# Performance work log

Hardware: AMD Instinct MI355X
Metric: run time of the kernel (lower is better)

Reference implementation:

```python
import jax, jax.numpy as jnp
import numpy as np

B, L, Hp, N, E, Z, GC = 32, 512, 192, 512, 128, 64, 3
TEMP, ALPHA, EPS = 0.5, 0.5, 1e-10


def _reparam(k, mu, var):
    return mu + jax.random.normal(k, mu.shape, mu.dtype) * jnp.exp(0.5 * var)


def setup_inputs() -> dict:
    key = jax.random.key(0)
    ks = jax.random.split(key, 42)
    def W(i, shape):
        return jax.random.normal(ks[i], shape, jnp.float32) * 0.02
    return {
        "batch_x": jax.random.normal(ks[0], (B, L, N), jnp.float32),
        "time_x": jax.random.normal(ks[1], (B, L, 7), jnp.float32),
        "time_W": W(2, (7, E)), "time_b": W(3, (E,)),
        "gate_W": W(4, (L, N)), "gate_b": W(5, (N,)),
        "mu_t_W": W(6, (E, Z)), "mu_t_b": W(7, (Z,)),
        "var_t_W": W(8, (E, Z)), "var_t_b": W(9, (Z,)),
        "ser_W": W(10, (L, E)), "ser_b": W(11, (E,)),
        "mu_h_W": W(12, (E, Z)), "mu_h_b": W(13, (Z,)),
        "var_h_W": W(14, (E, Z)), "var_h_b": W(15, (Z,)),
        "wkey": W(16, (Z, 1)), "wquery": W(17, (Z, 1)),
        "mlp_W": W(18, (GC + 1, 1)), "mlp_b": W(19, (1,)),
        "mu_ht_W": W(20, (E, Z)), "mu_ht_b": W(21, (Z,)),
        "var_ht_W": W(22, (E, Z)), "var_ht_b": W(23, (Z,)),
        "inf_W": W(24, (Z, Z)), "inf_b": W(25, (Z,)),
        "mu_zt_W": W(26, (Z, Z)), "mu_zt_b": W(27, (Z,)),
        "var_zt_W": W(28, (Z, Z)), "var_zt_b": W(29, (Z,)),
        "fW1": W(30, (Z, E)), "fb1": W(31, (E,)),
        "fW2": W(32, (E, Hp)), "fb2": W(33, (Hp,)),
        "rW1": W(34, (Z, E)), "rb1": W(35, (E,)),
        "rW2": W(36, (E, L)), "rb2": W(37, (L,)),
        "is_eval": 1,
    }


def _forward(batch_x, time_x, time_W, time_b, gate_W, gate_b, mu_t_W, mu_t_b,
             var_t_W, var_t_b, ser_W, ser_b, mu_h_W, mu_h_b, var_h_W, var_h_b,
             wkey, wquery, mlp_W, mlp_b, mu_ht_W, mu_ht_b, var_ht_W, var_ht_b,
             inf_W, inf_b, mu_zt_W, mu_zt_b, var_zt_W, var_zt_b,
             fW1, fb1, fW2, fb2, rW1, rb1, rW2, rb2):
    kz1, kz2, kg = jax.random.split(jax.random.key(42), 3)
    # TimeFeatureEmbedding + gate_layer_0 (Linear over the L axis)
    t = time_x @ time_W + time_b                                   # [B,L,E]
    t = jnp.einsum('ble,ln->bne', t, gate_W) + gate_b[None, :, None]  # [B,N,E]
    mu_t = t @ mu_t_W + mu_t_b
    var_t = t @ var_t_W + var_t_b
    # SeriesEmbedding: per-series Linear L->E, fused with time embedding
    h = jnp.einsum('bln,le->bne', batch_x, ser_W) + ser_b          # [B,N,E]
    h_hat = h + t
    mu_h_hat = h_hat @ mu_h_W + mu_h_b
    var_h_hat = h_hat @ var_h_W + var_h_b
    z_hat = _reparam(kz1, mu_h_hat, var_h_hat)                     # [B,N,Z]
    # self_graph_attention: key/query outer-sum -> leakyrelu -> softmax
    ksc = (z_hat @ wkey)[..., 0]                                   # [B,N]
    qsc = (z_hat @ wquery)[..., 0]
    att = jax.nn.softmax(jax.nn.leaky_relu(ksc[:, :, None] + qsc[:, None, :], 0.2), axis=-1)
    # (dropout identity in eval mode)
    lg = (att + 1.0) / 2.0                                         # [B,N,N]
    lg2 = jnp.stack([lg, 1.0 - lg], axis=-1).reshape(N * N, -1)    # [N*N, 2B] (faithful torch reshape)
    g = -jnp.log(-jnp.log(jax.random.uniform(kg, lg2.shape, lg2.dtype) + EPS) + EPS)
    soft = jax.nn.softmax((lg2 + g) / TEMP, axis=-1)
    hard = jax.nn.one_hot(jnp.argmax(soft, axis=-1), soft.shape[-1], dtype=soft.dtype)
    adj = (jax.lax.stop_gradient(hard - soft) + soft)[:, 0].reshape(N, N)
    adj = adj * (1.0 - jnp.eye(N, dtype=adj.dtype))                # masked_fill diagonal
    # graph_convolution: einsum('bnd,nn->bnd') takes the DIAGONAL of adj (faithful)
    diag = jnp.diagonal(adj)
    Hc, outs = h_hat, [h_hat]
    for _ in range(GC):
        Hc = Hc * diag[None, :, None]
        outs.append(Hc)
    h_tilde = (jnp.stack(outs, axis=-1) @ mlp_W + mlp_b)[..., 0]   # [B,N,E]
    mu_ht = h_tilde @ mu_ht_W + mu_ht_b
    var_ht = h_tilde @ var_ht_W + var_ht_b
    z_tilde = _reparam(kz2, mu_ht, var_ht)
    z = ALPHA * z_hat + (1.0 - ALPHA) * z_tilde
    mu_z = ALPHA * mu_h_hat + (1.0 - ALPHA) * mu_ht
    var_z = ALPHA * var_h_hat + (1.0 - ALPHA) * var_ht
    zt = z @ inf_W + inf_b
    mu_zt = zt @ mu_zt_W + mu_zt_b
    var_zt = zt @ var_zt_W + var_zt_b
    y = jnp.transpose((jax.nn.leaky_relu(z @ fW1 + fb1, 0.01) + h) @ fW2 + fb2, (0, 2, 1))  # [B,H,N]
    x = jnp.transpose((jax.nn.leaky_relu(z @ rW1 + rb1, 0.01) + h) @ rW2 + rb2, (0, 2, 1))  # [B,L,N]
    return (x, y, mu_t, var_t, mu_zt, var_zt, mu_z, var_z)


def reference(batch_x, time_x, time_W, time_b, gate_W, gate_b, mu_t_W, mu_t_b,
              var_t_W, var_t_b, ser_W, ser_b, mu_h_W, mu_h_b, var_h_W, var_h_b,
              wkey, wquery, mlp_W, mlp_b, mu_ht_W, mu_ht_b, var_ht_W, var_ht_b,
              inf_W, inf_b, mu_zt_W, mu_zt_b, var_zt_W, var_zt_b,
              fW1, fb1, fW2, fb2, rW1, rb1, rW2, rb2, is_eval):
    # is_eval: both branches of discrete_graph call gumbel_softmax(hard=True)
    return _forward(batch_x, time_x, time_W, time_b, gate_W, gate_b, mu_t_W, mu_t_b,
                    var_t_W, var_t_b, ser_W, ser_b, mu_h_W, mu_h_b, var_h_W, var_h_b,
                    wkey, wquery, mlp_W, mlp_b, mu_ht_W, mu_ht_b, var_ht_W, var_ht_b,
                    inf_W, inf_b, mu_zt_W, mu_zt_b, var_zt_W, var_zt_b,
                    fW1, fb1, fW2, fb2, rW1, rb1, rW2, rb2)
```

## Files before the change

### kernel.cpp

```cpp
#include <hip/hip_runtime.h>
#include <cstdint>
#include <cstddef>

#define B_ 32
#define L_ 512
#define HP_ 192
#define N_ 512
#define E_ 128
#define Z_ 64

typedef short bf16x8 __attribute__((ext_vector_type(8)));
typedef float f32x4 __attribute__((ext_vector_type(4)));

__host__ __device__ __forceinline__ uint32_t rotl32(uint32_t v, int r) {
    return (v << r) | (v >> (32 - r));
}

__host__ __device__ __forceinline__ void tf2x32(uint32_t k0, uint32_t k1,
                                                uint32_t c0, uint32_t c1,
                                                uint32_t& o0, uint32_t& o1) {
    uint32_t ks2 = k0 ^ k1 ^ 0x1BD11BDAu;
    uint32_t x0 = c0 + k0, x1 = c1 + k1;
    x0 += x1; x1 = rotl32(x1, 13); x1 ^= x0;
    x0 += x1; x1 = rotl32(x1, 15); x1 ^= x0;
    x0 += x1; x1 = rotl32(x1, 26); x1 ^= x0;
    x0 += x1; x1 = rotl32(x1, 6);  x1 ^= x0;
    x0 += k1; x1 += ks2 + 1u;
    x0 += x1; x1 = rotl32(x1, 17); x1 ^= x0;
    x0 += x1; x1 = rotl32(x1, 29); x1 ^= x0;
    x0 += x1; x1 = rotl32(x1, 16); x1 ^= x0;
    x0 += x1; x1 = rotl32(x1, 24); x1 ^= x0;
    x0 += ks2; x1 += k0 + 2u;
    x0 += x1; x1 = rotl32(x1, 13); x1 ^= x0;
    x0 += x1; x1 = rotl32(x1, 15); x1 ^= x0;
    x0 += x1; x1 = rotl32(x1, 26); x1 ^= x0;
    x0 += x1; x1 = rotl32(x1, 6);  x1 ^= x0;
    x0 += k0; x1 += k1 + 3u;
    x0 += x1; x1 = rotl32(x1, 17); x1 ^= x0;
    x0 += x1; x1 = rotl32(x1, 29); x1 ^= x0;
    x0 += x1; x1 = rotl32(x1, 16); x1 ^= x0;
    x0 += x1; x1 = rotl32(x1, 24); x1 ^= x0;
    x0 += k1; x1 += ks2 + 4u;
    x0 += x1; x1 = rotl32(x1, 13); x1 ^= x0;
    x0 += x1; x1 = rotl32(x1, 15); x1 ^= x0;
    x0 += x1; x1 = rotl32(x1, 26); x1 ^= x0;
    x0 += x1; x1 = rotl32(x1, 6);  x1 ^= x0;
    x0 += ks2; x1 += k0 + 5u;
    o0 = x0; o1 = x1;
}

__device__ __forceinline__ float erfinv_f(float x) {
    float w = -log1pf(-x * x);
    float p;
    if (w < 5.0f) {
        w = w - 2.5f;
        p = 2.81022636e-08f;
        p = fmaf(p, w, 3.43273939e-07f);
        p = fmaf(p, w, -3.5233877e-06f);
        p = fmaf(p, w, -4.39150654e-06f);
        p = fmaf(p, w, 0.00021858087f);
        p = fmaf(p, w, -0.00125372503f);
        p = fmaf(p, w, -0.00417768164f);
        p = fmaf(p, w, 0.246640727f);
        p = fmaf(p, w, 1.50140941f);
    } else {
        w = sqrtf(w) - 3.0f;
        p = -0.000200214257f;
        p = fmaf(p, w, 0.000100950558f);
        p = fmaf(p, w, 0.00134934322f);
        p = fmaf(p, w, -0.00367342844f);
        p = fmaf(p, w, 0.00573950773f);
        p = fmaf(p, w, -0.0076224613f);
        p = fmaf(p, w, 0.00943887047f);
        p = fmaf(p, w, 1.00167406f);
        p = fmaf(p, w, 2.83297682f);
    }
    return p * x;
}

__device__ __forceinline__ float bits_to_normal(uint32_t bits) {
    float f = __uint_as_float((bits >> 9) | 0x3f800000u) - 1.0f;
    const float lo = -0.99999994f;
    float u = fmaxf(lo, f * 2.0f + lo);
    return 1.41421354f * erfinv_f(u);
}

__device__ __forceinline__ uint32_t f2bf1(float x) {
    uint32_t u = __float_as_uint(x);
    return (u + 0x7fffu + ((u >> 16) & 1u)) >> 16;
}
__device__ __forceinline__ uint32_t f2bf2(float lo, float hi) {
    return f2bf1(lo) | (f2bf1(hi) << 16);
}

union U4BF8 { uint4 u; bf16x8 v; };

#define PO_WT   0
#define PO_WH   16384
#define PO_WI   49152
#define PO_WZZ  53248
#define PO_W1F  61440
#define PO_W1R  69632
#define PO_W2F  77824
#define PO_W2R  102400

struct PrepSrcs { const float* p[13]; };

__global__ void k_prep(PrepSrcs S, short* pool) {
    static const int Kt[13]  = {128,128,128,128,128,128,64,64,64,64,64,128,128};
    static const int Nst[13] = {64,64,64,64,64,64,64,64,64,128,128,192,512};
    static const int Ndt[13] = {128,128,256,256,256,256,64,128,128,128,128,192,512};
    static const int c0t[13] = {0,64,0,64,128,192,0,0,64,0,0,0,0};
    static const int offt[13]= {PO_WT,PO_WT,PO_WH,PO_WH,PO_WH,PO_WH,PO_WI,
                                PO_WZZ,PO_WZZ,PO_W1F,PO_W1R,PO_W2F,PO_W2R};
    int j = blockIdx.y;
    int Ns = Nst[j];
    int total = Kt[j] * Ns;
    int idx = blockIdx.x * 256 + threadIdx.x;
    if (idx >= total) return;
    int k = idx / Ns, nc = idx - k * Ns;
    float v = S.p[j][idx];
    int kc = k >> 5, k32 = k & 31;
    int fg = (k32 >> 2) & 3, e = (k32 & 3) + ((k32 >> 4) << 2);
    pool[offt[j] + (size_t)((kc * 4 + fg) * Ndt[j] + c0t[j] + nc) * 8 + e] = (short)f2bf1(v);
}

__global__ void k_pack(const float* __restrict__ gW, const float* __restrict__ sW,
                       const float* __restrict__ tx, const float* __restrict__ tW,
                       const float* __restrict__ tb,
                       const float* __restrict__ mW, const float* __restrict__ vW,
                       short* __restrict__ gfp, short* __restrict__ swp,
                       short* __restrict__ t0p, float* __restrict__ csum) {
    int mode = blockIdx.y;
    int idx = blockIdx.x * 256 + threadIdx.x;
    if (mode == 0) {
        if (idx >= 32768) return;
        int n = idx & 511, r = idx >> 9;
        int kc = r >> 2, fg = r & 3;
        int lb = kc * 32 + fg * 4;
        float v[8];
#pragma unroll
        for (int j = 0; j < 8; ++j)
            v[j] = gW[(size_t)(lb + (j & 3) + ((j >> 2) << 4)) * N_ + n];
        U4BF8 u;
        u.u.x = f2bf2(v[0], v[1]); u.u.y = f2bf2(v[2], v[3]);
        u.u.z = f2bf2(v[4], v[5]); u.u.w = f2bf2(v[6], v[7]);
        *(uint4*)&gfp[(size_t)((((n >> 5) * 16 + kc) * 4 + fg) * 32 + (n & 31)) * 8] = u.u;
    } else if (mode == 1) {
        if (idx >= 8192) return;
        int e = idx & 127, r = idx >> 7;
        int kc = r >> 2, fg = r & 3;
        int lb = kc * 32 + fg * 4;
        float v[8];
#pragma unroll
        for (int j = 0; j < 8; ++j)
            v[j] = sW[(size_t)(lb + (j & 3) + ((j >> 2) << 4)) * E_ + e];
        U4BF8 u;
        u.u.x = f2bf2(v[0], v[1]); u.u.y = f2bf2(v[2], v[3]);
        u.u.z = f2bf2(v[4], v[5]); u.u.w = f2bf2(v[6], v[7]);
        *(uint4*)&swp[(size_t)(r * 128 + e) * 8] = u.u;
    } else if (mode == 2) {
        if (idx >= 262144) return;
        int e = idx & 127, r2 = idx >> 7;
        int b = r2 >> 6, kf = r2 & 63;
        int kc = kf >> 2, fg = kf & 3;
        int lb = kc * 32 + fg * 4;
        float tbe = tb[e];
        float twc[7];
#pragma unroll
        for (int k = 0; k < 7; ++k) twc[k] = tW[k * E_ + e];
        float v[8];
#pragma unroll
        for (int j = 0; j < 8; ++j) {
            int l = lb + (j & 3) + ((j >> 2) << 4);
            const float* txr = &tx[((size_t)b * L_ + l) * 7];
            float a = tbe;
#pragma unroll
            for (int k = 0; k < 7; ++k) a = fmaf(txr[k], twc[k], a);
            v[j] = a;
        }
        U4BF8 u;
        u.u.x = f2bf2(v[0], v[1]); u.u.y = f2bf2(v[2], v[3]);
        u.u.z = f2bf2(v[4], v[5]); u.u.w = f2bf2(v[6], v[7]);
        *(uint4*)&t0p[(size_t)(r2 * 128 + e) * 8] = u.u;
    } else {
        if (idx >= 128) return;
        const float* W = (idx < 64) ? mW : vW;
        int zc = idx & 63;
        float s = 0.0f;
        for (int e = 0; e < E_; ++e) s += W[e * Z_ + zc];
        csum[idx] = s;
    }
}

__global__ __launch_bounds__(256) void k_gate4(
    const float* __restrict__ bx,
    const short* __restrict__ gfp, const short* __restrict__ swp,
    const short* __restrict__ t0p,
    const float* __restrict__ gb, const float* __restrict__ sb,
    float* __restrict__ t, float* __restrict__ h, float* __restrict__ hh) {
    const int ntile = blockIdx.x, eh = blockIdx.y, b = blockIdx.z;
    const int tid = threadIdx.x, lane = tid & 63, wv = tid >> 6;
    const int mw = wv & 1, ew = wv >> 1;
    const int fm = lane & 15, fl = lane >> 4;
    const int n0 = ntile * 32;
    const int e0 = eh * 64 + ew * 32;
    const int n = n0 + mw * 16 + fm;
    const float* bxp = &bx[(size_t)b * L_ * N_ + n];

    const f32x4 z4 = {0.f, 0.f, 0.f, 0.f};
    f32x4 accT[2] = {z4, z4}, accH[2] = {z4, z4};

    for (int kc = 0; kc < 16; ++kc) {
        int lb = kc * 32 + fl * 4;
        float xv[8];
#pragma unroll
        for (int j = 0; j < 8; ++j)
            xv[j] = bxp[(size_t)(lb + (j & 3) + ((j >> 2) << 4)) * N_];
        U4BF8 ux;
        ux.u.x = f2bf2(xv[0], xv[1]); ux.u.y = f2bf2(xv[2], xv[3]);
        ux.u.z = f2bf2(xv[4], xv[5]); ux.u.w = f2bf2(xv[6], xv[7]);
        bf16x8 fbx = ux.v;
        bf16x8 fgw = *(const bf16x8*)&gfp[(size_t)(((ntile * 16 + kc) * 4 + fl) * 32 + mw * 16 + fm) * 8];
#pragma unroll
        for (int nt = 0; nt < 2; ++nt) {
            int ec = e0 + nt * 16 + fm;
            bf16x8 ft = *(const bf16x8*)&t0p[(size_t)(((b * 16 + kc) * 4 + fl) * 128 + ec) * 8];
            bf16x8 fs = *(const bf16x8*)&swp[(size_t)((kc * 4 + fl) * 128 + ec) * 8];
            accT[nt] = __builtin_amdgcn_mfma_f32_16x16x32_bf16(fgw, ft, accT[nt], 0, 0, 0);
            accH[nt] = __builtin_amdgcn_mfma_f32_16x16x32_bf16(fbx, fs, accH[nt], 0, 0, 0);
        }
    }
    float gbn[4];
#pragma unroll
    for (int r = 0; r < 4; ++r) gbn[r] = gb[n0 + mw * 16 + fl * 4 + r];
#pragma unroll
    for (int nt = 0; nt < 2; ++nt) {
        int e = e0 + nt * 16 + fm;
        float sbe = sb[e];
#pragma unroll
        for (int r = 0; r < 4; ++r) {
            int nr = n0 + mw * 16 + fl * 4 + r;
            size_t base = ((size_t)b * N_ + nr) * E_ + e;
            float tv = accT[nt][r] + gbn[r];
            float hv = accH[nt][r] + sbe;
            t[base] = tv; h[base] = hv; hh[base] = tv + hv;
        }
    }
}

__global__ __launch_bounds__(256) void k_mega2(
    const float* __restrict__ T, const float* __restrict__ HH,
    const float* __restrict__ h,
    const short* __restrict__ pool,
    const float* __restrict__ bmt_, const float* __restrict__ bvt_,
    const float* __restrict__ bmh, const float* __restrict__ bvh,
    const float* __restrict__ bmht, const float* __restrict__ bvht,
    const float* __restrict__ mlpW, const float* __restrict__ mlpb,
    const float* __restrict__ csum,
    const float* __restrict__ ib,
    const float* __restrict__ mzb, const float* __restrict__ vzb,
    const float* __restrict__ fb1, const float* __restrict__ rb1,
    float* __restrict__ Omt, float* __restrict__ Ovt,
    float* __restrict__ Omz, float* __restrict__ Ovz,
    float* __restrict__ Omzt, float* __restrict__ Ovzt,
    float* __restrict__ tmpF, float* __restrict__ tmpR,
    uint32_t k1a, uint32_t k1b, uint32_t k2a, uint32_t k2b) {
    __shared__ __align__(16) short sAT[4 * 4 * 32 * 8];
    __shared__ __align__(16) short sAH[4 * 4 * 32 * 8];
    __shared__ __align__(16) short sZf[2 * 4 * 32 * 8];
    __shared__ __align__(16) short sZTf[2 * 4 * 32 * 8];
    __shared__ float sOut[32][260];

    const short* Wt  = pool + PO_WT;
    const short* Wh  = pool + PO_WH;
    const short* Wi  = pool + PO_WI;
    const short* Wzz = pool + PO_WZZ;
    const short* W1f = pool + PO_W1F;
    const short* W1r = pool + PO_W1R;

    const int r0 = blockIdx.x * 32;
    const int tid = threadIdx.x;
    const int lane = tid & 63, wv = tid >> 6;
    const int fm = lane & 15, flane = lane >> 4;
    const int m = wv & 1, nb = wv >> 1;
    const f32x4 z4 = {0.f, 0.f, 0.f, 0.f};

#pragma unroll
    for (int it = 0; it < 4; ++it) {
        int idx = tid + it * 256;
        int row = idx >> 5, c4 = idx & 31;
        int k0 = c4 * 4;
        int kc = k0 >> 5, k32 = k0 & 31;
        int fg = (k32 >> 2) & 3, e0 = (k32 >= 16) ? 4 : 0;
        int base = ((kc * 4 + fg) * 32 + row) * 8 + e0;
        float4 v = *(const float4*)&T[(size_t)(r0 + row) * E_ + k0];
        uint2 u; u.x = f2bf2(v.x, v.y); u.y = f2bf2(v.z, v.w);
        *(uint2*)&sAT[base] = u;
        float4 w = *(const float4*)&HH[(size_t)(r0 + row) * E_ + k0];
        uint2 p; p.x = f2bf2(w.x, w.y); p.y = f2bf2(w.z, w.w);
        *(uint2*)&sAH[base] = p;
    }
    __syncthreads();

    {
        bf16x8 fa[4];
#pragma unroll
        for (int kc = 0; kc < 4; ++kc)
            fa[kc] = *(const bf16x8*)&sAT[((kc * 4 + flane) * 32 + m * 16 + fm) * 8];
        f32x4 acc[4] = {z4, z4, z4, z4};
#pragma unroll
        for (int j = 0; j < 4; ++j) {
            int nt = nb + 2 * j;
#pragma unroll
            for (int kc = 0; kc < 4; ++kc) {
                bf16x8 fb = *(const bf16x8*)&Wt[(size_t)((kc * 4 + flane) * 128 + nt * 16 + fm) * 8];
                acc[j] = __builtin_amdgcn_mfma_f32_16x16x32_bf16(fa[kc], fb, acc[j], 0, 0, 0);
            }
        }
#pragma unroll
        for (int j = 0; j < 4; ++j) {
            int ncol = (nb + 2 * j) * 16 + fm;
            float* dst = (ncol < 64) ? Omt : Ovt;
            int zc = ncol & 63;
            float bias = (ncol < 64) ? bmt_[zc] : bvt_[zc];
#pragma unroll
            for (int r = 0; r < 4; ++r) {
                int row = m * 16 + flane * 4 + r;
                dst[(size_t)(r0 + row) * Z_ + zc] = acc[j][r] + bias;
            }
        }
    }

    {
        bf16x8 fa[4];
#pragma unroll
        for (int kc = 0; kc < 4; ++kc)
            fa[kc] = *(const bf16x8*)&sAH[((kc * 4 + flane) * 32 + m * 16 + fm) * 8];
        f32x4 acc[8] = {z4, z4, z4, z4, z4, z4, z4, z4};
#pragma unroll
        for (int j = 0; j < 8; ++j) {
            int nt = nb + 2 * j;
#pragma unroll
            for (int kc = 0; kc < 4; ++kc) {
                bf16x8 fb = *(const bf16x8*)&Wh[(size_t)((kc * 4 + flane) * 256 + nt * 16 + fm) * 8];
                acc[j] = __builtin_amdgcn_mfma_f32_16x16x32_bf16(fa[kc], fb, acc[j], 0, 0, 0);
            }
        }
#pragma unroll
        for (int j = 0; j < 8; ++j) {
            int ncol = (nb + 2 * j) * 16 + fm;
#pragma unroll
            for (int r = 0; r < 4; ++r)
                sOut[m * 16 + flane * 4 + r][ncol] = acc[j][r];
        }
    }
    __syncthreads();

    {
        float w0 = mlpW[0], b0 = mlpb[0];
        int row = tid >> 3;
        int zc0 = (tid & 7) * 8;
        int r = r0 + row;
        float zm[8], zvv[8];
        uint32_t zb[8];
#pragma unroll
        for (int j = 0; j < 8; ++j) {
            int zc = zc0 + j;
            float m1 = sOut[row][zc] + bmh[zc];
            float v1 = sOut[row][64 + zc] + bvh[zc];
            float m2 = fmaf(w0, sOut[row][128 + zc], fmaf(b0, csum[zc], bmht[zc]));
            float v2 = fmaf(w0, sOut[row][192 + zc], fmaf(b0, csum[64 + zc], bvht[zc]));
            uint32_t flat = (uint32_t)r * 64u + (uint32_t)zc;
            uint32_t o0, o1;
            tf2x32(k1a, k1b, 0u, flat, o0, o1);
            float e1 = bits_to_normal(o0 ^ o1);
            tf2x32(k2a, k2b, 0u, flat, o0, o1);
            float e2 = bits_to_normal(o0 ^ o1);
            float zh = m1 + e1 * expf(0.5f * v1);
            float zt = m2 + e2 * expf(0.5f * v2);
            float zval = 0.5f * (zh + zt);
            zb[j] = f2bf1(zval);
            zm[j] = 0.5f * (m1 + m2);
            zvv[j] = 0.5f * (v1 + v2);
        }
        size_t base = (size_t)r * Z_ + zc0;
        *(float4*)&Omz[base]     = make_float4(zm[0], zm[1], zm[2], zm[3]);
        *(float4*)&Omz[base + 4] = make_float4(zm[4], zm[5], zm[6], zm[7]);
        *(float4*)&Ovz[base]     = make_float4(zvv[0], zvv[1], zvv[2], zvv[3]);
        *(float4*)&Ovz[base + 4] = make_float4(zvv[4], zvv[5], zvv[6], zvv[7]);
        int kc = zc0 >> 5, z32 = zc0 & 31;
        int fgA = (z32 >> 2) & 3, eA = (z32 >= 16) ? 4 : 0;
        uint2 u;
        u.x = zb[0] | (zb[1] << 16); u.y = zb[2] | (zb[3] << 16);
        *(uint2*)&sZf[((kc * 4 + fgA) * 32 + row) * 8 + eA] = u;
        u.x = zb[4] | (zb[5] << 16); u.y = zb[6] | (zb[7] << 16);
        *(uint2*)&sZf[((kc * 4 + fgA + 1) * 32 + row) * 8 + eA] = u;
    }
    __syncthreads();

    {
        bf16x8 fa[2];
#pragma unroll
        for (int kc = 0; kc < 2; ++kc)
            fa[kc] = *(const bf16x8*)&sZf[((kc * 4 + flane) * 32 + m * 16 + fm) * 8];
        f32x4 acc[2] = {z4, z4};
#pragma unroll
        for (int j = 0; j < 2; ++j) {
            int nt = nb + 2 * j;
#pragma unroll
            for (int kc = 0; kc < 2; ++kc) {
                bf16x8 fb = *(const bf16x8*)&Wi[(size_t)((kc * 4 + flane) * 64 + nt * 16 + fm) * 8];
                acc[j] = __builtin_amdgcn_mfma_f32_16x16x32_bf16(fa[kc], fb, acc[j], 0, 0, 0);
            }
        }
#pragma unroll
        for (int j = 0; j < 2; ++j) {
            int col = (nb + 2 * j) * 16 + fm;
            float bias = ib[col];
            int kc2 = col >> 5, c32 = col & 31;
            int fg2 = (c32 >> 2) & 3, e2 = (c32 & 3) + ((c32 >> 4) << 2);
#pragma unroll
            for (int r = 0; r < 4; ++r) {
                int row2 = m * 16 + flane * 4 + r;
                sZTf[((kc2 * 4 + fg2) * 32 + row2) * 8 + e2] = (short)f2bf1(acc[j][r] + bias);
            }
        }
    }
    __syncthreads();

    {
        bf16x8 fa[2];
#pragma unroll
        for (int kc = 0; kc < 2; ++kc)
            fa[kc] = *(const bf16x8*)&sZTf[((kc * 4 + flane) * 32 + m * 16 + fm) * 8];
        f32x4 acc[4] = {z4, z4, z4, z4};
#pragma unroll
        for (int j = 0; j < 4; ++j) {
            int nt = nb + 2 * j;
#pragma unroll
            for (int kc = 0; kc < 2; ++kc) {
                bf16x8 fb = *(const bf16x8*)&Wzz[(size_t)((kc * 4 + flane) * 128 + nt * 16 + fm) * 8];
                acc[j] = __builtin_amdgcn_mfma_f32_16x16x32_bf16(fa[kc], fb, acc[j], 0, 0, 0);
            }
        }
#pragma unroll
        for (int j = 0; j < 4; ++j) {
            int ncol = (nb + 2 * j) * 16 + fm;
            float* dst = (ncol < 64) ? Omzt : Ovzt;
            int zc = ncol & 63;
            float bias = (ncol < 64) ? mzb[zc] : vzb[zc];
#pragma unroll
            for (int r = 0; r < 4; ++r) {
                int row = m * 16 + flane * 4 + r;
                dst[(size_t)(r0 + row) * Z_ + zc] = acc[j][r] + bias;
            }
        }
    }

    {
        bf16x8 fa[2];
#pragma unroll
        for (int kc = 0; kc < 2; ++kc)
            fa[kc] = *(const bf16x8*)&sZf[((kc * 4 + flane) * 32 + m * 16 + fm) * 8];
#pragma unroll
        for (int head = 0; head < 2; ++head) {
            const short* W1 = head ? W1r : W1f;
            const float* b1 = head ? rb1 : fb1;
            float* outp = head ? tmpR : tmpF;
            f32x4 acc[4] = {z4, z4, z4, z4};
#pragma unroll
            for (int j = 0; j < 4; ++j) {
                int nt = nb + 2 * j;
#pragma unroll
                for (int kc = 0; kc < 2; ++kc) {
                    bf16x8 fb = *(const bf16x8*)&W1[(size_t)((kc * 4 + flane) * 128 + nt * 16 + fm) * 8];
                    acc[j] = __builtin_amdgcn_mfma_f32_16x16x32_bf16(fa[kc], fb, acc[j], 0, 0, 0);
                }
            }
#pragma unroll
            for (int j = 0; j < 4; ++j) {
                int col = (nb + 2 * j) * 16 + fm;
                float bias = b1[col];
#pragma unroll
                for (int r = 0; r < 4; ++r) {
                    int row = m * 16 + flane * 4 + r;
                    size_t gi = (size_t)(r0 + row) * E_ + col;
                    float v = acc[j][r] + bias;
                    v = (v > 0.0f) ? v : 0.01f * v;
                    outp[gi] = v + h[gi];
                }
            }
        }
    }
}

__global__ __launch_bounds__(256) void k_out_mfma(
    const float* __restrict__ tmp, const short* __restrict__ Wpack,
    const float* __restrict__ b2, float* __restrict__ out, int Dout) {
    __shared__ __align__(16) short sB[4 * 4 * 64 * 8];
    const int r0 = blockIdx.x * 64;
    const int d0 = blockIdx.y * 64;
    const int b = r0 >> 9, nbase = r0 & 511;
    const int tid = threadIdx.x, lane = tid & 63, wave = tid >> 6;
    const int fm = lane & 15, fg = lane >> 4;
    const int col = tid & 63, sg = tid >> 6;
#pragma unroll
    for (int kc = 0; kc < 4; ++kc) {
        float4 b0 = *(const float4*)&tmp[(size_t)(r0 + col) * E_ + kc * 32 + sg * 4];
        float4 b1 = *(const float4*)&tmp[(size_t)(r0 + col) * E_ + kc * 32 + 16 + sg * 4];
        uint4 v;
        v.x = f2bf2(b0.x, b0.y); v.y = f2bf2(b0.z, b0.w);
        v.z = f2bf2(b1.x, b1.y); v.w = f2bf2(b1.z, b1.w);
        *(uint4*)&sB[((kc * 4 + sg) * 64 + col) * 8] = v;
    }
    __syncthreads();
    const f32x4 zv = {0.f, 0.f, 0.f, 0.f};
    f32x4 acc[4] = {zv, zv, zv, zv};
#pragma unroll
    for (int kc = 0; kc < 4; ++kc) {
        bf16x8 fa = *(const bf16x8*)&Wpack[(size_t)((kc * 4 + fg) * Dout + d0 + wave * 16 + fm) * 8];
#pragma unroll
        for (int nt = 0; nt < 4; ++nt) {
            bf16x8 fb = *(const bf16x8*)&sB[((kc * 4 + fg) * 64 + nt * 16 + fm) * 8];
            acc[nt] = __builtin_amdgcn_mfma_f32_16x16x32_bf16(fa, fb, acc[nt], 0, 0, 0);
        }
    }
#pragma unroll
    for (int r = 0; r < 4; ++r) {
        int d = d0 + wave * 16 + fg * 4 + r;
        float bb = b2[d];
#pragma unroll
        for (int nt = 0; nt < 4; ++nt) {
            int n = nbase + nt * 16 + fm;
            out[((size_t)b * Dout + d) * N_ + n] = acc[nt][r] + bb;
        }
    }
}

extern "C" void kernel_launch(void* const* d_in, const int* in_sizes, int n_in,
                              void* d_out, int out_size, void* d_ws, size_t ws_size,
                              hipStream_t stream) {
    (void)in_sizes; (void)n_in; (void)out_size; (void)ws_size;
    const float* batch_x = (const float*)d_in[0];
    const float* time_x  = (const float*)d_in[1];
    const float* time_W  = (const float*)d_in[2];
    const float* time_b  = (const float*)d_in[3];
    const float* gate_W  = (const float*)d_in[4];
    const float* gate_b  = (const float*)d_in[5];
    const float* mu_t_W  = (const float*)d_in[6];
    const float* mu_t_b  = (const float*)d_in[7];
    const float* var_t_W = (const float*)d_in[8];
    const float* var_t_b = (const float*)d_in[9];
    const float* ser_W   = (const float*)d_in[10];
    const float* ser_b   = (const float*)d_in[11];
    const float* mu_h_W  = (const float*)d_in[12];
    const float* mu_h_b  = (const float*)d_in[13];
    const float* var_h_W = (const float*)d_in[14];
    const float* var_h_b = (const float*)d_in[15];
    const float* mlp_W   = (const float*)d_in[18];
    const float* mlp_b   = (const float*)d_in[19];
    const float* mu_ht_W = (const float*)d_in[20];
    const float* mu_ht_b = (const float*)d_in[21];
    const float* var_ht_W = (const float*)d_in[22];
    const float* var_ht_b = (const float*)d_in[23];
    const float* inf_W   = (const float*)d_in[24];
    const float* inf_b   = (const float*)d_in[25];
    const float* mu_zt_W = (const float*)d_in[26];
    const float* mu_zt_b = (const float*)d_in[27];
    const float* var_zt_W = (const float*)d_in[28];
    const float* var_zt_b = (const float*)d_in[29];
    const float* fW1 = (const float*)d_in[30];
    const float* fb1 = (const float*)d_in[31];
    const float* fW2 = (const float*)d_in[32];
    const float* fb2 = (const float*)d_in[33];
    const float* rW1 = (const float*)d_in[34];
    const float* rb1 = (const float*)d_in[35];
    const float* rW2 = (const float*)d_in[36];
    const float* rb2 = (const float*)d_in[37];

    float* out = (float*)d_out;
    float* ws = (float*)d_ws;

    const size_t off_t0p  = 0;
    const size_t off_pool = 1048576;
    const size_t off_gfp  = 1245184;
    const size_t off_swp  = 1376256;
    const size_t off_t    = 2097152;
    const size_t off_tmpF = 2097152;
    const size_t off_h    = 4194304;
    const size_t off_hh   = 6291456;
    const size_t off_tmpR = 6291456;
    const size_t off_csum = 8388608;

    short* pool = (short*)(ws + off_pool);
    short* gfp  = (short*)(ws + off_gfp);
    short* swp  = (short*)(ws + off_swp);
    short* t0p  = (short*)(ws + off_t0p);

    float* o_x     = out;
    float* o_y     = out + 8388608;
    float* o_mu_t  = out + 11534336;
    float* o_var_t = out + 12582912;
    float* o_mu_zt = out + 13631488;
    float* o_var_zt= out + 14680064;
    float* o_mu_z  = out + 15728640;
    float* o_var_z = out + 16777216;

    uint32_t kz1a, kz1b, kz2a, kz2b;
    tf2x32(0u, 42u, 0u, 0u, kz1a, kz1b);
    tf2x32(0u, 42u, 0u, 1u, kz2a, kz2b);

    PrepSrcs S;
    S.p[0] = mu_t_W;  S.p[1] = var_t_W;
    S.p[2] = mu_h_W;  S.p[3] = var_h_W; S.p[4] = mu_ht_W; S.p[5] = var_ht_W;
    S.p[6] = inf_W;   S.p[7] = mu_zt_W; S.p[8] = var_zt_W;
    S.p[9] = fW1;     S.p[10] = rW1;    S.p[11] = fW2;    S.p[12] = rW2;

    k_prep<<<dim3(256, 13), 256, 0, stream>>>(S, pool);
    k_pack<<<dim3(1024, 4), 256, 0, stream>>>(gate_W, ser_W, time_x, time_W, time_b,
                                              mu_ht_W, var_ht_W,
                                              gfp, swp, t0p, ws + off_csum);
    k_gate4<<<dim3(16, 2, B_), 256, 0, stream>>>(batch_x, gfp, swp, t0p,
                                                 gate_b, ser_b,
                                                 ws + off_t, ws + off_h, ws + off_hh);
    k_mega2<<<512, 256, 0, stream>>>(ws + off_t, ws + off_hh, ws + off_h, pool,
                                     mu_t_b, var_t_b, mu_h_b, var_h_b,
                                     mu_ht_b, var_ht_b, mlp_W, mlp_b,
                                     ws + off_csum, inf_b, mu_zt_b, var_zt_b,
                                     fb1, rb1,
                                     o_mu_t, o_var_t, o_mu_z, o_var_z,
                                     o_mu_zt, o_var_zt,
                                     ws + off_tmpF, ws + off_tmpR,
                                     kz1a, kz1b, kz2a, kz2b);
    k_out_mfma<<<dim3(256, HP_ / 64), 256, 0, stream>>>(ws + off_tmpF, pool + PO_W2F,
                                                        fb2, o_y, HP_);
    k_out_mfma<<<dim3(256, L_ / 64), 256, 0, stream>>>(ws + off_tmpR, pool + PO_W2R,
                                                       rb2, o_x, L_);
}
```

Before: 245.1 us.

## Fuse output projections into mega kernel and merge weight prep into pack kernel

The second-layer projections for y and x are now computed inside the main per-row kernel. The intermediate activations are kept as bf16 in shared memory (reusing the sOut buffer) instead of being written to global scratch and re-read by two separate k_out_mfma launches. The weight-prep kernel is also folded into k_pack as extra grid rows, which removes a launch. In exchange, each mega block does much more serial MFMA work with only 512 blocks, adds several __syncthreads, and reads the W2 weights per block from global memory without LDS staging.

```diff
diff --git a/kernel.cpp b/kernel.cpp
--- a/kernel.cpp
+++ b/kernel.cpp
@@ -106,31 +106,19 @@
 
 struct PrepSrcs { const float* p[13]; };
 
-__global__ void k_prep(PrepSrcs S, short* pool) {
+__global__ void k_pack(PrepSrcs S, short* __restrict__ pool,
+                       const float* __restrict__ gW, const float* __restrict__ sW,
+                       const float* __restrict__ tx, const float* __restrict__ tW,
+                       const float* __restrict__ tb,
+                       const float* __restrict__ mW, const float* __restrict__ vW,
+                       short* __restrict__ gfp, short* __restrict__ swp,
+                       short* __restrict__ t0p, float* __restrict__ csum) {
     static const int Kt[13]  = {128,128,128,128,128,128,64,64,64,64,64,128,128};
     static const int Nst[13] = {64,64,64,64,64,64,64,64,64,128,128,192,512};
     static const int Ndt[13] = {128,128,256,256,256,256,64,128,128,128,128,192,512};
     static const int c0t[13] = {0,64,0,64,128,192,0,0,64,0,0,0,0};
     static const int offt[13]= {PO_WT,PO_WT,PO_WH,PO_WH,PO_WH,PO_WH,PO_WI,
                                 PO_WZZ,PO_WZZ,PO_W1F,PO_W1R,PO_W2F,PO_W2R};
-    int j = blockIdx.y;
-    int Ns = Nst[j];
-    int total = Kt[j] * Ns;
-    int idx = blockIdx.x * 256 + threadIdx.x;
-    if (idx >= total) return;
-    int k = idx / Ns, nc = idx - k * Ns;
-    float v = S.p[j][idx];
-    int kc = k >> 5, k32 = k & 31;
-    int fg = (k32 >> 2) & 3, e = (k32 & 3) + ((k32 >> 4) << 2);
-    pool[offt[j] + (size_t)((kc * 4 + fg) * Ndt[j] + c0t[j] + nc) * 8 + e] = (short)f2bf1(v);
-}
-
-__global__ void k_pack(const float* __restrict__ gW, const float* __restrict__ sW,
-                       const float* __restrict__ tx, const float* __restrict__ tW,
-                       const float* __restrict__ tb,
-                       const float* __restrict__ mW, const float* __restrict__ vW,
-                       short* __restrict__ gfp, short* __restrict__ swp,
-                       short* __restrict__ t0p, float* __restrict__ csum) {
     int mode = blockIdx.y;
     int idx = blockIdx.x * 256 + threadIdx.x;
     if (mode == 0) {
@@ -183,13 +171,23 @@
         u.u.x = f2bf2(v[0], v[1]); u.u.y = f2bf2(v[2], v[3]);
         u.u.z = f2bf2(v[4], v[5]); u.u.w = f2bf2(v[6], v[7]);
         *(uint4*)&t0p[(size_t)(r2 * 128 + e) * 8] = u.u;
-    } else {
+    } else if (mode == 3) {
         if (idx >= 128) return;
         const float* W = (idx < 64) ? mW : vW;
         int zc = idx & 63;
         float s = 0.0f;
         for (int e = 0; e < E_; ++e) s += W[e * Z_ + zc];
         csum[idx] = s;
+    } else {
+        int j = mode - 4;
+        int Ns = Nst[j];
+        int total = Kt[j] * Ns;
+        if (idx >= total) return;
+        int k = idx / Ns, nc = idx - k * Ns;
+        float v = S.p[j][idx];
+        int kc = k >> 5, k32 = k & 31;
+        int fg = (k32 >> 2) & 3, e = (k32 & 3) + ((k32 >> 4) << 2);
+        pool[offt[j] + (size_t)((kc * 4 + fg) * Ndt[j] + c0t[j] + nc) * 8 + e] = (short)f2bf1(v);
     }
 }
 
@@ -249,7 +247,7 @@
     }
 }
 
-__global__ __launch_bounds__(256) void k_mega2(
+__global__ __launch_bounds__(256) void k_mega3(
     const float* __restrict__ T, const float* __restrict__ HH,
     const float* __restrict__ h,
     const short* __restrict__ pool,
@@ -261,16 +259,18 @@
     const float* __restrict__ ib,
     const float* __restrict__ mzb, const float* __restrict__ vzb,
     const float* __restrict__ fb1, const float* __restrict__ rb1,
+    const float* __restrict__ fb2, const float* __restrict__ rb2,
     float* __restrict__ Omt, float* __restrict__ Ovt,
     float* __restrict__ Omz, float* __restrict__ Ovz,
     float* __restrict__ Omzt, float* __restrict__ Ovzt,
-    float* __restrict__ tmpF, float* __restrict__ tmpR,
+    float* __restrict__ Oy, float* __restrict__ Ox,
     uint32_t k1a, uint32_t k1b, uint32_t k2a, uint32_t k2b) {
     __shared__ __align__(16) short sAT[4 * 4 * 32 * 8];
     __shared__ __align__(16) short sAH[4 * 4 * 32 * 8];
     __shared__ __align__(16) short sZf[2 * 4 * 32 * 8];
     __shared__ __align__(16) short sZTf[2 * 4 * 32 * 8];
-    __shared__ float sOut[32][260];
+    __shared__ __align__(16) float sOut[32][260];
+    short* sTmp = (short*)&sOut[0][0];
 
     const short* Wt  = pool + PO_WT;
     const short* Wh  = pool + PO_WH;
@@ -278,8 +278,11 @@
     const short* Wzz = pool + PO_WZZ;
     const short* W1f = pool + PO_W1F;
     const short* W1r = pool + PO_W1R;
+    const short* W2f = pool + PO_W2F;
+    const short* W2r = pool + PO_W2R;
 
     const int r0 = blockIdx.x * 32;
+    const int bb = r0 >> 9, nbase = r0 & 511;
     const int tid = threadIdx.x;
     const int lane = tid & 63, wv = tid >> 6;
     const int fm = lane & 15, flane = lane >> 4;
@@ -384,6 +387,7 @@
             zm[j] = 0.5f * (m1 + m2);
             zvv[j] = 0.5f * (v1 + v2);
         }
+        __syncthreads();
         size_t base = (size_t)r * Z_ + zc0;
         *(float4*)&Omz[base]     = make_float4(zm[0], zm[1], zm[2], zm[3]);
         *(float4*)&Omz[base + 4] = make_float4(zm[4], zm[5], zm[6], zm[7]);
@@ -463,77 +467,104 @@
 #pragma unroll
         for (int kc = 0; kc < 2; ++kc)
             fa[kc] = *(const bf16x8*)&sZf[((kc * 4 + flane) * 32 + m * 16 + fm) * 8];
-#pragma unroll
-        for (int head = 0; head < 2; ++head) {
-            const short* W1 = head ? W1r : W1f;
-            const float* b1 = head ? rb1 : fb1;
-            float* outp = head ? tmpR : tmpF;
+
+        {
             f32x4 acc[4] = {z4, z4, z4, z4};
 #pragma unroll
             for (int j = 0; j < 4; ++j) {
                 int nt = nb + 2 * j;
 #pragma unroll
                 for (int kc = 0; kc < 2; ++kc) {
-                    bf16x8 fb = *(const bf16x8*)&W1[(size_t)((kc * 4 + flane) * 128 + nt * 16 + fm) * 8];
+                    bf16x8 fb = *(const bf16x8*)&W1f[(size_t)((kc * 4 + flane) * 128 + nt * 16 + fm) * 8];
                     acc[j] = __builtin_amdgcn_mfma_f32_16x16x32_bf16(fa[kc], fb, acc[j], 0, 0, 0);
                 }
             }
 #pragma unroll
             for (int j = 0; j < 4; ++j) {
                 int col = (nb + 2 * j) * 16 + fm;
-                float bias = b1[col];
+                float bias = fb1[col];
 #pragma unroll
                 for (int r = 0; r < 4; ++r) {
                     int row = m * 16 + flane * 4 + r;
-                    size_t gi = (size_t)(r0 + row) * E_ + col;
                     float v = acc[j][r] + bias;
                     v = (v > 0.0f) ? v : 0.01f * v;
-                    outp[gi] = v + h[gi];
+                    v += h[(size_t)(r0 + row) * E_ + col];
+                    sTmp[((j * 4 + (fm >> 2)) * 32 + row) * 8 + (fm & 3) + 4 * nb] = (short)f2bf1(v);
                 }
             }
         }
-    }
-}
-
-__global__ __launch_bounds__(256) void k_out_mfma(
-    const float* __restrict__ tmp, const short* __restrict__ Wpack,
-    const float* __restrict__ b2, float* __restrict__ out, int Dout) {
-    __shared__ __align__(16) short sB[4 * 4 * 64 * 8];
-    const int r0 = blockIdx.x * 64;
-    const int d0 = blockIdx.y * 64;
-    const int b = r0 >> 9, nbase = r0 & 511;
-    const int tid = threadIdx.x, lane = tid & 63, wave = tid >> 6;
-    const int fm = lane & 15, fg = lane >> 4;
-    const int col = tid & 63, sg = tid >> 6;
-#pragma unroll
-    for (int kc = 0; kc < 4; ++kc) {
-        float4 b0 = *(const float4*)&tmp[(size_t)(r0 + col) * E_ + kc * 32 + sg * 4];
-        float4 b1 = *(const float4*)&tmp[(size_t)(r0 + col) * E_ + kc * 32 + 16 + sg * 4];
-        uint4 v;
-        v.x = f2bf2(b0.x, b0.y); v.y = f2bf2(b0.z, b0.w);
-        v.z = f2bf2(b1.x, b1.y); v.w = f2bf2(b1.z, b1.w);
-        *(uint4*)&sB[((kc * 4 + sg) * 64 + col) * 8] = v;
-    }
-    __syncthreads();
-    const f32x4 zv = {0.f, 0.f, 0.f, 0.f};
-    f32x4 acc[4] = {zv, zv, zv, zv};
-#pragma unroll
-    for (int kc = 0; kc < 4; ++kc) {
-        bf16x8 fa = *(const bf16x8*)&Wpack[(size_t)((kc * 4 + fg) * Dout + d0 + wave * 16 + fm) * 8];
-#pragma unroll
-        for (int nt = 0; nt < 4; ++nt) {
-            bf16x8 fb = *(const bf16x8*)&sB[((kc * 4 + fg) * 64 + nt * 16 + fm) * 8];
-            acc[nt] = __builtin_amdgcn_mfma_f32_16x16x32_bf16(fa, fb, acc[nt], 0, 0, 0);
-        }
-    }
-#pragma unroll
-    for (int r = 0; r < 4; ++r) {
-        int d = d0 + wave * 16 + fg * 4 + r;
-        float bb = b2[d];
-#pragma unroll
-        for (int nt = 0; nt < 4; ++nt) {
-            int n = nbase + nt * 16 + fm;
-            out[((size_t)b * Dout + d) * N_ + n] = acc[nt][r] + bb;
+        __syncthreads();
+        {
+            int d0w = wv * 48;
+#pragma unroll
+            for (int ntile = 0; ntile < 2; ++ntile) {
+                f32x4 acc2[3] = {z4, z4, z4};
+#pragma unroll
+                for (int dt = 0; dt < 3; ++dt)
+#pragma unroll
+                    for (int kc = 0; kc < 4; ++kc) {
+                        bf16x8 fA = *(const bf16x8*)&W2f[(size_t)((kc * 4 + flane) * HP_ + d0w + dt * 16 + fm) * 8];
+                        bf16x8 fB = *(const bf16x8*)&sTmp[((kc * 4 + flane) * 32 + ntile * 16 + fm) * 8];
+                        acc2[dt] = __builtin_amdgcn_mfma_f32_16x16x32_bf16(fA, fB, acc2[dt], 0, 0, 0);
+                    }
+#pragma unroll
+                for (int dt = 0; dt < 3; ++dt)
+#pragma unroll
+                    for (int r = 0; r < 4; ++r) {
+                        int d = d0w + dt * 16 + flane * 4 + r;
+                        Oy[((size_t)bb * HP_ + d) * N_ + nbase + ntile * 16 + fm] = acc2[dt][r] + fb2[d];
+                    }
+            }
+        }
+        __syncthreads();
+
+        {
+            f32x4 acc[4] = {z4, z4, z4, z4};
+#pragma unroll
+            for (int j = 0; j < 4; ++j) {
+                int nt = nb + 2 * j;
+#pragma unroll
+                for (int kc = 0; kc < 2; ++kc) {
+                    bf16x8 fb = *(const bf16x8*)&W1r[(size_t)((kc * 4 + flane) * 128 + nt * 16 + fm) * 8];
+                    acc[j] = __builtin_amdgcn_mfma_f32_16x16x32_bf16(fa[kc], fb, acc[j], 0, 0, 0);
+                }
+            }
+#pragma unroll
+            for (int j = 0; j < 4; ++j) {
+                int col = (nb + 2 * j) * 16 + fm;
+                float bias = rb1[col];
+#pragma unroll
+                for (int r = 0; r < 4; ++r) {
+                    int row = m * 16 + flane * 4 + r;
+                    float v = acc[j][r] + bias;
+                    v = (v > 0.0f) ? v : 0.01f * v;
+                    v += h[(size_t)(r0 + row) * E_ + col];
+                    sTmp[((j * 4 + (fm >> 2)) * 32 + row) * 8 + (fm & 3) + 4 * nb] = (short)f2bf1(v);
+                }
+            }
+        }
+        __syncthreads();
+        {
+            int d0w = wv * 128;
+#pragma unroll
+            for (int ntile = 0; ntile < 2; ++ntile) {
+                f32x4 acc2[8] = {z4, z4, z4, z4, z4, z4, z4, z4};
+#pragma unroll
+                for (int dt = 0; dt < 8; ++dt)
+#pragma unroll
+                    for (int kc = 0; kc < 4; ++kc) {
+                        bf16x8 fA = *(const bf16x8*)&W2r[(size_t)((kc * 4 + flane) * L_ + d0w + dt * 16 + fm) * 8];
+                        bf16x8 fB = *(const bf16x8*)&sTmp[((kc * 4 + flane) * 32 + ntile * 16 + fm) * 8];
+                        acc2[dt] = __builtin_amdgcn_mfma_f32_16x16x32_bf16(fA, fB, acc2[dt], 0, 0, 0);
+                    }
+#pragma unroll
+                for (int dt = 0; dt < 8; ++dt)
+#pragma unroll
+                    for (int r = 0; r < 4; ++r) {
+                        int d = d0w + dt * 16 + flane * 4 + r;
+                        Ox[((size_t)bb * L_ + d) * N_ + nbase + ntile * 16 + fm] = acc2[dt][r] + rb2[d];
+                    }
+            }
         }
     }
 }
@@ -587,10 +618,8 @@
     const size_t off_gfp  = 1245184;
     const size_t off_swp  = 1376256;
     const size_t off_t    = 2097152;
-    const size_t off_tmpF = 2097152;
     const size_t off_h    = 4194304;
     const size_t off_hh   = 6291456;
-    const size_t off_tmpR = 6291456;
     const size_t off_csum = 8388608;
 
     short* pool = (short*)(ws + off_pool);
@@ -617,24 +646,20 @@
     S.p[6] = inf_W;   S.p[7] = mu_zt_W; S.p[8] = var_zt_W;
     S.p[9] = fW1;     S.p[10] = rW1;    S.p[11] = fW2;    S.p[12] = rW2;
 
-    k_prep<<<dim3(256, 13), 256, 0, stream>>>(S, pool);
-    k_pack<<<dim3(1024, 4), 256, 0, stream>>>(gate_W, ser_W, time_x, time_W, time_b,
-                                              mu_ht_W, var_ht_W,
-                                              gfp, swp, t0p, ws + off_csum);
+    k_pack<<<dim3(1024, 17), 256, 0, stream>>>(S, pool, gate_W, ser_W,
+                                               time_x, time_W, time_b,
+                                               mu_ht_W, var_ht_W,
+                                               gfp, swp, t0p, ws + off_csum);
     k_gate4<<<dim3(16, 2, B_), 256, 0, stream>>>(batch_x, gfp, swp, t0p,
                                                  gate_b, ser_b,
                                                  ws + off_t, ws + off_h, ws + off_hh);
-    k_mega2<<<512, 256, 0, stream>>>(ws + off_t, ws + off_hh, ws + off_h, pool,
+    k_mega3<<<512, 256, 0, stream>>>(ws + off_t, ws + off_hh, ws + off_h, pool,
                                      mu_t_b, var_t_b, mu_h_b, var_h_b,
                                      mu_ht_b, var_ht_b, mlp_W, mlp_b,
                                      ws + off_csum, inf_b, mu_zt_b, var_zt_b,
-                                     fb1, rb1,
+                                     fb1, rb1, fb2, rb2,
                                      o_mu_t, o_var_t, o_mu_z, o_var_z,
                                      o_mu_zt, o_var_zt,
-                                     ws + off_tmpF, ws + off_tmpR,
+                                     o_y, o_x,
                                      kz1a, kz1b, kz2a, kz2b);
-    k_out_mfma<<<dim3(256, HP_ / 64), 256, 0, stream>>>(ws + off_tmpF, pool + PO_W2F,
-                                                        fb2, o_y, HP_);
-    k_out_mfma<<<dim3(256, L_ / 64), 256, 0, stream>>>(ws + off_tmpR, pool + PO_W2R,
-                                                       rb2, o_x, L_);
-}
+}
```

Measured after the change: 243.5 us. About the same (-0.6%).
